# Kernel tuning notes

Measured on AMD Instinct MI355X. Metric: run time of the kernel, lower is better.

The kernel has to match this reference:

```python
import jax, jax.numpy as jnp
import numpy as np

B, L = 1024, 1024
NCAT, NNUM = 20, 10
CAT_BUCKETS, SEQ_VOCAB = 100000, 50000
E, A, H, QH = 32, 128, 256, 256
TOPK = 30


def _init(key, shape, scale=0.02):
    return scale * jax.random.normal(key, shape, dtype=jnp.float32)


def setup_inputs() -> dict:
    key = jax.random.key(0)
    ks = jax.random.split(key, 24)
    z = lambda *s: jnp.zeros(s, dtype=jnp.float32)
    return {
        "cats": jax.random.randint(ks[0], (B, NCAT), 0, CAT_BUCKETS + 1),
        "nums": jax.random.normal(ks[1], (B, NNUM), dtype=jnp.float32),
        "seqs": jax.random.randint(ks[2], (B, L), 0, SEQ_VOCAB + 1),
        "tgt_ids": jax.random.randint(ks[3], (B,), 0, CAT_BUCKETS + 1),
        "cat_emb": _init(ks[4], (CAT_BUCKETS + 1, E)),
        "seq_emb": _init(ks[5], (SEQ_VOCAB + 1, E)),
        "Wnum": _init(ks[6], (NNUM, E)), "bnum": z(E),
        "Wq": _init(ks[7], (E, A)), "Wk": _init(ks[8], (E, A)), "Wv": _init(ks[9], (E, A)),
        "Wo": _init(ks[10], (A, E)), "bo": z(E),
        "Wpool": _init(ks[11], (NCAT * E, E)), "bpool": z(E),
        "Wmlp": _init(ks[12], (4 * E, H)), "bmlp": z(H),
        "q1_W1": _init(ks[13], (H, QH)), "q1_b1": z(QH),
        "q1_W2": _init(ks[14], (H, QH)), "q1_b2": z(QH),
        "q1_Wp": _init(ks[15], (QH, H)), "q1_bp": z(H),
        "q2_W1": _init(ks[16], (H, QH)), "q2_b1": z(QH),
        "q2_W2": _init(ks[17], (H, QH)), "q2_b2": z(QH),
        "q2_Wp": _init(ks[18], (QH, H)), "q2_bp": z(H),
        "Wout": _init(ks[19], (H, 1)), "bout": z(1),
    }


def _qnn(x, W1, b1, W2, b2, Wp, bp):
    # Quadratic neural block (QIN-style): Hadamard product of two linear maps,
    # projected back with a residual connection. Dropout is identity in eval.
    quad = (x @ W1 + b1) * (x @ W2 + b2)
    return x + quad @ Wp + bp


def reference(cats, nums, seqs, tgt_ids, cat_emb, seq_emb, Wnum, bnum, Wq, Wk, Wv,
              Wo, bo, Wpool, bpool, Wmlp, bmlp,
              q1_W1, q1_b1, q1_W2, q1_b2, q1_Wp, q1_bp,
              q2_W1, q2_b1, q2_W2, q2_b2, q2_Wp, q2_bp, Wout, bout):
    cat_e = cat_emb[cats]                                   # [B, NCAT, E]
    cat_pool = cat_e.reshape(cat_e.shape[0], -1) @ Wpool + bpool   # [B, E]
    num_e = nums @ Wnum + bnum                              # [B, E]
    tgt_e = cat_emb[tgt_ids]                                # [B, E] (tgt_emb shares cat_emb)
    seq_e = seq_emb[seqs]                                   # [B, L, E]

    q = tgt_e @ Wq                                          # [B, A]
    k = seq_e @ Wk                                          # [B, L, A]
    v = seq_e @ Wv                                          # [B, L, A]
    scores = jnp.einsum('ba,bla->bl', q, k) / jnp.sqrt(jnp.float32(A))

    # top-k + scatter mask + masked softmax == softmax over the top-k scores,
    # scattered implicitly via gather of the selected values.
    vals, idx = jax.lax.top_k(scores, TOPK)                 # [B, TOPK]
    w = jax.nn.softmax(vals, axis=1)                        # [B, TOPK]
    v_sel = jnp.take_along_axis(v, idx[:, :, None], axis=1)  # [B, TOPK, A]
    interest = jnp.einsum('bk,bka->ba', w, v_sel) @ Wo + bo  # [B, E]

    fused = jnp.concatenate([tgt_e, interest, cat_pool, num_e], axis=1)  # [B, 4E]
    h = jax.nn.relu(fused @ Wmlp + bmlp)                    # [B, H], dropout=eval
    h = _qnn(h, q1_W1, q1_b1, q1_W2, q1_b2, q1_Wp, q1_bp)
    h = _qnn(h, q2_W1, q2_b1, q2_W2, q2_b2, q2_Wp, q2_bp)
    return (h @ Wout + bout)[:, 0]                          # [B]
```

## Files before the change

kernel.cpp:

```cpp
#include <hip/hip_runtime.h>
#include <hip/hip_fp16.h>

#define B_ 1024
#define L_ 1024
#define NCAT_ 20
#define NNUM_ 10
#define E_ 32
#define A_ 128
#define H_ 256
#define TOPK_ 30
#define INV_SQRT_A 0.08838834764831845f

typedef _Float16 half8 __attribute__((ext_vector_type(8)));
typedef float f32x4 __attribute__((ext_vector_type(4)));

__device__ __forceinline__ unsigned sortable(float f) {
    unsigned u = __float_as_uint(f);
    return (u & 0x80000000u) ? ~u : (u | 0x80000000u);
}
__device__ __forceinline__ float unsortable(unsigned s) {
    unsigned u = (s & 0x80000000u) ? (s ^ 0x80000000u) : ~s;
    return __uint_as_float(u);
}
__device__ __forceinline__ half8 cvt_h8(const float4 u, const float4 v) {
    half8 a;
    a[0] = (_Float16)u.x; a[1] = (_Float16)u.y;
    a[2] = (_Float16)u.z; a[3] = (_Float16)u.w;
    a[4] = (_Float16)v.x; a[5] = (_Float16)v.y;
    a[6] = (_Float16)v.z; a[7] = (_Float16)v.w;
    return a;
}

#define K1_GRID 1356
__global__ __launch_bounds__(256) void fused_prep_kernel(
    const int* __restrict__ cats, const float* __restrict__ nums,
    const int* __restrict__ tgt_ids, const float* __restrict__ cat_emb,
    const float* __restrict__ Wnum, const float* __restrict__ bnum,
    const float* __restrict__ Wq, const float* __restrict__ Wk,
    const float* __restrict__ Wv, const float* __restrict__ Wo,
    const float* __restrict__ Wpool, const float* __restrict__ bpool,
    const float* __restrict__ seq_emb, const float* __restrict__ Wmlp,
    const float* __restrict__ q1W1, const float* __restrict__ q1W2,
    const float* __restrict__ q1Wp,
    const float* __restrict__ q2W1, const float* __restrict__ q2W2,
    const float* __restrict__ q2Wp,
    float* __restrict__ p_out, float* __restrict__ fused, float* __restrict__ M,
    __half2* __restrict__ seq_h2,
    __half* __restrict__ WmlpT,
    __half* __restrict__ W1T1, __half* __restrict__ W2T1, __half* __restrict__ WpT1,
    __half* __restrict__ W1T2, __half* __restrict__ W2T2, __half* __restrict__ WpT2)
{
    const int blk = blockIdx.x;
    const int t = threadIdx.x;

    if (blk < 256) {
        __shared__ float ce[4][NCAT_ * E_];
        __shared__ float tg[4][E_];
        __shared__ float nm[4][NNUM_];
        __shared__ float qs[4][A_];
        __shared__ float part[8][4][E_];
        const int r0 = blk * 4;

        for (int idx = t; idx < 640; idx += 256) {
            const int q = idx >> 3, f4 = idx & 7;
            const int row = q / 20, cat = q % 20;
            const int tok = cats[(r0 + row) * NCAT_ + cat];
            ((float4*)&ce[row][cat * 32])[f4] =
                ((const float4*)(cat_emb + (size_t)tok * 32))[f4];
        }
        if (t < 32) {
            const int row = t >> 3, f4 = t & 7;
            const int tok = tgt_ids[r0 + row];
            ((float4*)&tg[row][0])[f4] =
                ((const float4*)(cat_emb + (size_t)tok * 32))[f4];
        }
        if (t >= 64 && t < 104) {
            const int x = t - 64;
            nm[x / 10][x % 10] = nums[(r0 + x / 10) * NNUM_ + x % 10];
        }
        __syncthreads();

        {
            const int w = t >> 6, lane = t & 63;
            float q0 = 0.f, q1 = 0.f;
#pragma unroll
            for (int e = 0; e < E_; ++e) {
                float te = tg[w][e];
                q0 += te * Wq[e * A_ + lane];
                q1 += te * Wq[e * A_ + lane + 64];
            }
            qs[w][lane] = q0; qs[w][lane + 64] = q1;
        }

        {
            const int iseg = t >> 5;
            const int row = (t >> 3) & 3;
            const int c0 = (t & 7) * 4;
            float4 acc = make_float4(0.f, 0.f, 0.f, 0.f);
            const int i0 = iseg * 80;
            for (int i = i0; i < i0 + 80; ++i) {
                float4 wv = *(const float4*)(Wpool + i * 32 + c0);
                acc.x += ce[row][i] * wv.x; acc.y += ce[row][i] * wv.y;
                acc.z += ce[row][i] * wv.z; acc.w += ce[row][i] * wv.w;
            }
            *(float4*)&part[iseg][row][c0] = acc;
        }
        __syncthreads();

        if (t < 128) {
            const int row = t >> 5, c = t & 31;
            const int b = r0 + row;
            float s = bpool[c];
#pragma unroll
            for (int g = 0; g < 8; ++g) s += part[g][row][c];
            fused[b * 128 + 64 + c] = s;
            fused[b * 128 + c] = tg[row][c];

            float ne = bnum[c];
#pragma unroll
            for (int n = 0; n < NNUM_; ++n) ne += nm[row][n] * Wnum[n * 32 + c];
            fused[b * 128 + 96 + c] = ne;

            float pv = 0.f;
#pragma unroll 8
            for (int a = 0; a < A_; ++a) pv += Wk[c * A_ + a] * qs[row][a];
            p_out[b * 32 + c] = pv;
        }
        return;
    }

    if (blk < 1280) {
        int x = (blk - 256) * 256 + t;
        for (; x < 800016; x += 1024 * 256) {
            float2 v = ((const float2*)seq_emb)[x];
            seq_h2[x] = __float22half2_rn(v);
        }
        return;
    }

    if (blk < 1284) {
        const int o = (blk - 1280) * 256 + t;
        const int j = o >> 5, e = o & 31;
        float sm = 0.f;
#pragma unroll 8
        for (int a = 0; a < A_; ++a) sm += Wv[j * A_ + a] * Wo[a * E_ + e];
        M[o] = sm;
        return;
    }

    {
        int c = (blk - 1284) * 256 + t;
        for (; c < 53248; c += 72 * 256) {
            const float* src; __half* dst;
            int n, k0, K;
            if (c < 4096) {
                n = c >> 4; k0 = (c & 15) << 3; K = 128;
                src = Wmlp; dst = WmlpT;
            } else {
                const int c2 = c - 4096;
                const int m = c2 >> 13, idx = c2 & 8191;
                n = idx >> 5; k0 = (idx & 31) << 3; K = 256;
                switch (m) {
                    case 0: src = q1W1; dst = W1T1; break;
                    case 1: src = q1W2; dst = W2T1; break;
                    case 2: src = q1Wp; dst = WpT1; break;
                    case 3: src = q2W1; dst = W1T2; break;
                    case 4: src = q2W2; dst = W2T2; break;
                    default: src = q2Wp; dst = WpT2; break;
                }
            }
            float v[8];
#pragma unroll
            for (int i = 0; i < 8; ++i) v[i] = src[(size_t)(k0 + i) * 256 + n];
            float4 wq;
            __half2* hp = (__half2*)&wq;
            hp[0] = __float22half2_rn(make_float2(v[0], v[1]));
            hp[1] = __float22half2_rn(make_float2(v[2], v[3]));
            hp[2] = __float22half2_rn(make_float2(v[4], v[5]));
            hp[3] = __float22half2_rn(make_float2(v[6], v[7]));
            *(float4*)(dst + (size_t)n * K + k0) = wq;
        }
    }
}

#define RM 2
__global__ __launch_bounds__(512) void score_topk_kernel(
    const int* __restrict__ seqs, const __half* __restrict__ seq_h,
    const float* __restrict__ seq_emb, const float* __restrict__ p,
    const float* __restrict__ M, const float* __restrict__ bo,
    float* __restrict__ fused)
{
    const int b0 = blockIdx.x * RM;
    const int tid = threadIdx.x;

    __shared__ float sc[RM][L_];
    __shared__ float ps[RM][E_];
    __shared__ float sw[RM][32];
    __shared__ int   stok[RM][32];

    if (tid < RM * 32)
        ps[tid >> 5][tid & 31] = p[(b0 + (tid >> 5)) * 32 + (tid & 31)];
    __syncthreads();

    {
        const int row = tid >> 8;
        const int s = tid & 255;
        const int bb = b0 + row;
#pragma unroll
        for (int jj = 0; jj < 2; ++jj) {
            const int l1 = jj * 512 + s;
            const int l2 = l1 + 256;
            const int tok1 = seqs[bb * L_ + l1];
            const int tok2 = seqs[bb * L_ + l2];
            float4 buf[2][4];
            const float4* r1 = (const float4*)(seq_h + (size_t)tok1 * 32);
            const float4* r2 = (const float4*)(seq_h + (size_t)tok2 * 32);
#pragma unroll
            for (int i = 0; i < 4; ++i) buf[0][i] = r1[i];
#pragma unroll
            for (int i = 0; i < 4; ++i) buf[1][i] = r2[i];

            float acc0 = 0.f, acc1 = 0.f;
#pragma unroll
            for (int i = 0; i < 4; ++i) {
                const __half2* h1 = (const __half2*)&buf[0][i];
                const __half2* h2 = (const __half2*)&buf[1][i];
#pragma unroll
                for (int u = 0; u < 4; ++u) {
                    float2 f1 = __half22float2(h1[u]);
                    float2 f2 = __half22float2(h2[u]);
                    acc0 += f1.x * ps[row][i * 8 + 2 * u] + f1.y * ps[row][i * 8 + 2 * u + 1];
                    acc1 += f2.x * ps[row][i * 8 + 2 * u] + f2.y * ps[row][i * 8 + 2 * u + 1];
                }
            }
            sc[row][l1] = acc0 * INV_SQRT_A;
            sc[row][l2] = acc1 * INV_SQRT_A;
        }
    }
    __syncthreads();

    if (tid < RM * 64) {
        const int w = tid >> 6;
        const int lane = tid & 63;
        const int bb = b0 + w;

        unsigned long long key[16];
#pragma unroll
        for (int j = 0; j < 16; ++j) {
            const int l = j * 64 + lane;
            key[j] = ((unsigned long long)sortable(sc[w][l]) << 10)
                   | (unsigned)(1023 - l);
        }
#pragma unroll
        for (int a = 0; a < 15; ++a)
#pragma unroll
            for (int j = 0; j < 15 - a; ++j) {
                const bool swp = key[j] < key[j + 1];
                const unsigned long long hi = swp ? key[j + 1] : key[j];
                const unsigned long long lo = swp ? key[j] : key[j + 1];
                key[j] = hi; key[j + 1] = lo;
            }

        float myv = -1e30f; int myl = 0;
        unsigned long long front = key[0];
        for (int k = 0; k < TOPK_; ++k) {
            unsigned long long wk = front;
#pragma unroll
            for (int off = 32; off > 0; off >>= 1) {
                unsigned long long o = __shfl_xor(wk, off);
                if (o > wk) wk = o;
            }
            if (lane == k) {
                myv = unsortable((unsigned)(wk >> 10));
                myl = 1023 - (int)(wk & 1023);
            }
            if (front == wk) {
#pragma unroll
                for (int j = 0; j < 15; ++j) key[j] = key[j + 1];
                key[15] = 0ULL;
                front = key[0];
            }
        }

        float m = myv;
#pragma unroll
        for (int off = 32; off > 0; off >>= 1) m = fmaxf(m, __shfl_xor(m, off));
        float e = (lane < TOPK_) ? expf(myv - m) : 0.f;
        float s = e;
#pragma unroll
        for (int off = 32; off > 0; off >>= 1) s += __shfl_xor(s, off);
        if (lane < TOPK_) {
            sw[w][lane]   = e / s;
            stok[w][lane] = seqs[bb * L_ + myl];
        }

        if (lane < E_) {
            float acc = 0.f;
#pragma unroll
            for (int k = 0; k < TOPK_; ++k)
                acc += sw[w][k] * seq_emb[(size_t)stok[w][k] * 32 + lane];
            sc[w][lane] = acc;
        }
        if (lane < E_) {
            float acc = bo[lane];
#pragma unroll
            for (int j = 0; j < E_; ++j) acc += sc[w][j] * M[j * E_ + lane];
            fused[bb * 128 + 32 + lane] = acc;
        }
    }
}

#define GR 16
#define HSP 260
#define TSP 264
__global__ __launch_bounds__(512) void mlp_mfma_kernel(
    const float* __restrict__ fused,
    const __half* __restrict__ WmlpT, const float* __restrict__ bmlp,
    const __half* __restrict__ W1T1, const __half* __restrict__ W2T1,
    const __half* __restrict__ WpT1,
    const float* __restrict__ b11, const float* __restrict__ b12,
    const float* __restrict__ b1p,
    const __half* __restrict__ W1T2, const __half* __restrict__ W2T2,
    const __half* __restrict__ WpT2,
    const float* __restrict__ b21, const float* __restrict__ b22,
    const float* __restrict__ b2p,
    const float* __restrict__ Wout, const float* __restrict__ bout,
    float* __restrict__ out)
{
    const int r0 = blockIdx.x * GR;
    const int tid = threadIdx.x;
    const int w = tid >> 6;
    const int l = tid & 63;
    const int lr = l & 15;
    const int lk = l >> 4;
    const int n0 = w * 32;

    __shared__ float hs[GR][HSP];
    __shared__ __half ts_h[GR][TSP];

    f32x4 hC0, hC1;
    const f32x4 zf = {0.f, 0.f, 0.f, 0.f};

    {
        half8 ax[4];
        const float* xrow = fused + (size_t)(r0 + lr) * 128 + lk * 8;
#pragma unroll
        for (int ks = 0; ks < 4; ++ks) {
            float4 u = *(const float4*)(xrow + ks * 32);
            float4 v = *(const float4*)(xrow + ks * 32 + 4);
            ax[ks] = cvt_h8(u, v);
        }
#pragma unroll
        for (int t = 0; t < 2; ++t) {
            f32x4 c = zf;
            const __half* wb = WmlpT + (size_t)(n0 + 16 * t + lr) * 128 + lk * 8;
#pragma unroll
            for (int ks = 0; ks < 4; ++ks) {
                half8 b = *(const half8*)(wb + ks * 32);
                c = __builtin_amdgcn_mfma_f32_16x16x32_f16(ax[ks], b, c, 0, 0, 0);
            }
            const int j = n0 + 16 * t + lr;
            const float bm = bmlp[j];
#pragma unroll
            for (int r = 0; r < 4; ++r) {
                float vv = fmaxf(c[r] + bm, 0.f);
                if (t == 0) hC0[r] = vv; else hC1[r] = vv;
                hs[4 * lk + r][j] = vv;
            }
        }
    }
    __syncthreads();

#pragma unroll
    for (int q = 0; q < 2; ++q) {
        const __half* W1T = q ? W1T2 : W1T1;
        const __half* W2T = q ? W2T2 : W2T1;
        const __half* WpT = q ? WpT2 : WpT1;
        const float* bb1 = q ? b21 : b11;
        const float* bb2 = q ? b22 : b12;
        const float* bbp = q ? b2p : b1p;

        half8 ah[8];
#pragma unroll
        for (int ks = 0; ks < 8; ++ks) {
            const float* hr = &hs[lr][ks * 32 + lk * 8];
            float4 u = *(const float4*)hr;
            float4 v = *(const float4*)(hr + 4);
            ah[ks] = cvt_h8(u, v);
        }
#pragma unroll
        for (int t = 0; t < 2; ++t) {
            f32x4 t1 = zf, t2 = zf;
            const __half* w1 = W1T + (size_t)(n0 + 16 * t + lr) * 256 + lk * 8;
            const __half* w2 = W2T + (size_t)(n0 + 16 * t + lr) * 256 + lk * 8;
#pragma unroll
            for (int ks = 0; ks < 8; ++ks) {
                half8 b1 = *(const half8*)(w1 + ks * 32);
                t1 = __builtin_amdgcn_mfma_f32_16x16x32_f16(ah[ks], b1, t1, 0, 0, 0);
                half8 b2 = *(const half8*)(w2 + ks * 32);
                t2 = __builtin_amdgcn_mfma_f32_16x16x32_f16(ah[ks], b2, t2, 0, 0, 0);
            }
            const int j = n0 + 16 * t + lr;
            const float v1 = bb1[j], v2 = bb2[j];
#pragma unroll
            for (int r = 0; r < 4; ++r) {
                float tv = (t1[r] + v1) * (t2[r] + v2);
                ts_h[4 * lk + r][j] = __float2half_rn(tv);
            }
        }
        __syncthreads();

        half8 pa[8];
#pragma unroll
        for (int ks = 0; ks < 8; ++ks)
            pa[ks] = *(const half8*)&ts_h[lr][ks * 32 + lk * 8];
#pragma unroll
        for (int t = 0; t < 2; ++t) {
            f32x4 c = (t == 0) ? hC0 : hC1;
            const __half* wp = WpT + (size_t)(n0 + 16 * t + lr) * 256 + lk * 8;
#pragma unroll
            for (int ks = 0; ks < 8; ++ks) {
                half8 b = *(const half8*)(wp + ks * 32);
                c = __builtin_amdgcn_mfma_f32_16x16x32_f16(pa[ks], b, c, 0, 0, 0);
            }
            const int j = n0 + 16 * t + lr;
            const float bp = bbp[j];
#pragma unroll
            for (int r = 0; r < 4; ++r) {
                float vv = c[r] + bp;
                if (t == 0) hC0[r] = vv; else hC1[r] = vv;
                hs[4 * lk + r][j] = vv;
            }
        }
        __syncthreads();
    }

    {
        const int i = tid >> 5;
        const int seg = tid & 31;
        const int cb = seg * 8;
        float psum = 0.f;
#pragma unroll
        for (int u = 0; u < 8; ++u) psum += hs[i][cb + u] * Wout[cb + u];
#pragma unroll
        for (int off = 16; off > 0; off >>= 1) psum += __shfl_xor(psum, off);
        if (seg == 0) out[r0 + i] = psum + bout[0];
    }
}

extern "C" void kernel_launch(void* const* d_in, const int* in_sizes, int n_in,
                              void* d_out, int out_size, void* d_ws, size_t ws_size,
                              hipStream_t stream) {
    const int*   cats    = (const int*)d_in[0];
    const float* nums    = (const float*)d_in[1];
    const int*   seqs    = (const int*)d_in[2];
    const int*   tgt_ids = (const int*)d_in[3];
    const float* cat_emb = (const float*)d_in[4];
    const float* seq_emb = (const float*)d_in[5];
    const float* Wnum    = (const float*)d_in[6];
    const float* bnum    = (const float*)d_in[7];
    const float* Wq      = (const float*)d_in[8];
    const float* Wk      = (const float*)d_in[9];
    const float* Wv      = (const float*)d_in[10];
    const float* Wo      = (const float*)d_in[11];
    const float* bo      = (const float*)d_in[12];
    const float* Wpool   = (const float*)d_in[13];
    const float* bpool   = (const float*)d_in[14];
    const float* Wmlp    = (const float*)d_in[15];
    const float* bmlp    = (const float*)d_in[16];
    const float* q1_W1   = (const float*)d_in[17];
    const float* q1_b1   = (const float*)d_in[18];
    const float* q1_W2   = (const float*)d_in[19];
    const float* q1_b2   = (const float*)d_in[20];
    const float* q1_Wp   = (const float*)d_in[21];
    const float* q1_bp   = (const float*)d_in[22];
    const float* q2_W1   = (const float*)d_in[23];
    const float* q2_b1   = (const float*)d_in[24];
    const float* q2_W2   = (const float*)d_in[25];
    const float* q2_b2   = (const float*)d_in[26];
    const float* q2_Wp   = (const float*)d_in[27];
    const float* q2_bp   = (const float*)d_in[28];
    const float* Wout    = (const float*)d_in[29];
    const float* bout    = (const float*)d_in[30];

    float* ws = (float*)d_ws;
    float*   p       = ws;
    float*   fused   = ws + 32768;
    float*   M       = ws + 163840;
    __half2* seq_h2  = (__half2*)(ws + 164864);
    __half*  WmlpT   = (__half*)(ws + 964928);
    __half*  W1T1    = (__half*)(ws + 981312);
    __half*  W2T1    = (__half*)(ws + 1014080);
    __half*  WpT1    = (__half*)(ws + 1046848);
    __half*  W1T2    = (__half*)(ws + 1079616);
    __half*  W2T2    = (__half*)(ws + 1112384);
    __half*  WpT2    = (__half*)(ws + 1145152);

    float* out = (float*)d_out;

    fused_prep_kernel<<<K1_GRID, 256, 0, stream>>>(
        cats, nums, tgt_ids, cat_emb, Wnum, bnum, Wq, Wk, Wv, Wo,
        Wpool, bpool, seq_emb, Wmlp,
        q1_W1, q1_W2, q1_Wp, q2_W1, q2_W2, q2_Wp,
        p, fused, M, seq_h2,
        WmlpT, W1T1, W2T1, WpT1, W1T2, W2T2, WpT2);

    score_topk_kernel<<<B_ / RM, 512, 0, stream>>>(
        seqs, (const __half*)seq_h2, seq_emb, p, M, bo, fused);

    mlp_mfma_kernel<<<B_ / GR, 512, 0, stream>>>(
        fused, WmlpT, bmlp,
        W1T1, W2T1, WpT1, q1_b1, q1_b2, q1_bp,
        W1T2, W2T2, WpT2, q2_b1, q2_b2, q2_bp,
        Wout, bout, out);
}
```

Baseline: 200.6 us.

## Drop fp16 seq table conversion and fuse score/top-k with MLP via last-block counter

Removes the per-call fp32-to-fp16 conversion of the whole sequence embedding table and has the score kernel read fp32 rows directly. It also merges the score/top-k kernel with the MLP kernel: each group of four blocks increments an atomic counter, and the last block to arrive runs the MFMA MLP for its 16 rows. The intent is to avoid converting the full table when only the gathered rows are used, and to save one kernel launch. In exchange, gathers are now twice as wide, and the MLP runs on only a quarter of the blocks, serialized behind the counter.

New measurement: 219.1 us. +9.2%, slower.

```diff
diff --git a/kernel.cpp b/kernel.cpp
--- a/kernel.cpp
+++ b/kernel.cpp
@@ -31,7 +31,7 @@
     return a;
 }
 
-#define K1_GRID 1356
+#define K1_GRID 332
 __global__ __launch_bounds__(256) void fused_prep_kernel(
     const int* __restrict__ cats, const float* __restrict__ nums,
     const int* __restrict__ tgt_ids, const float* __restrict__ cat_emb,
@@ -39,13 +39,13 @@
     const float* __restrict__ Wq, const float* __restrict__ Wk,
     const float* __restrict__ Wv, const float* __restrict__ Wo,
     const float* __restrict__ Wpool, const float* __restrict__ bpool,
-    const float* __restrict__ seq_emb, const float* __restrict__ Wmlp,
+    const float* __restrict__ Wmlp,
     const float* __restrict__ q1W1, const float* __restrict__ q1W2,
     const float* __restrict__ q1Wp,
     const float* __restrict__ q2W1, const float* __restrict__ q2W2,
     const float* __restrict__ q2Wp,
     float* __restrict__ p_out, float* __restrict__ fused, float* __restrict__ M,
-    __half2* __restrict__ seq_h2,
+    int* __restrict__ cnt,
     __half* __restrict__ WmlpT,
     __half* __restrict__ W1T1, __half* __restrict__ W2T1, __half* __restrict__ WpT1,
     __half* __restrict__ W1T2, __half* __restrict__ W2T2, __half* __restrict__ WpT2)
@@ -76,7 +76,7 @@
         }
         if (t >= 64 && t < 104) {
             const int x = t - 64;
-            nm[x / 10][x % 10] = nums[(r0 + x / 10) * NNUM_ + x % 10];
+            nm[x / 10][x % 10] = nums[(x / 10) * 0 + (r0 + x / 10) * NNUM_ + x % 10];
         }
         __syncthreads();
 
@@ -129,17 +129,9 @@
         return;
     }
 
-    if (blk < 1280) {
-        int x = (blk - 256) * 256 + t;
-        for (; x < 800016; x += 1024 * 256) {
-            float2 v = ((const float2*)seq_emb)[x];
-            seq_h2[x] = __float22half2_rn(v);
-        }
-        return;
-    }
-
-    if (blk < 1284) {
-        const int o = (blk - 1280) * 256 + t;
+    if (blk < 260) {
+        if (blk == 256 && t < 64) cnt[t] = 0;
+        const int o = (blk - 256) * 256 + t;
         const int j = o >> 5, e = o & 31;
         float sm = 0.f;
 #pragma unroll 8
@@ -149,7 +141,7 @@
     }
 
     {
-        int c = (blk - 1284) * 256 + t;
+        int c = (blk - 260) * 256 + t;
         for (; c < 53248; c += 72 * 256) {
             const float* src; __half* dst;
             int n, k0, K;
@@ -183,138 +175,15 @@
     }
 }
 
-#define RM 2
-__global__ __launch_bounds__(512) void score_topk_kernel(
-    const int* __restrict__ seqs, const __half* __restrict__ seq_h,
-    const float* __restrict__ seq_emb, const float* __restrict__ p,
-    const float* __restrict__ M, const float* __restrict__ bo,
-    float* __restrict__ fused)
-{
-    const int b0 = blockIdx.x * RM;
-    const int tid = threadIdx.x;
-
-    __shared__ float sc[RM][L_];
-    __shared__ float ps[RM][E_];
-    __shared__ float sw[RM][32];
-    __shared__ int   stok[RM][32];
-
-    if (tid < RM * 32)
-        ps[tid >> 5][tid & 31] = p[(b0 + (tid >> 5)) * 32 + (tid & 31)];
-    __syncthreads();
-
-    {
-        const int row = tid >> 8;
-        const int s = tid & 255;
-        const int bb = b0 + row;
-#pragma unroll
-        for (int jj = 0; jj < 2; ++jj) {
-            const int l1 = jj * 512 + s;
-            const int l2 = l1 + 256;
-            const int tok1 = seqs[bb * L_ + l1];
-            const int tok2 = seqs[bb * L_ + l2];
-            float4 buf[2][4];
-            const float4* r1 = (const float4*)(seq_h + (size_t)tok1 * 32);
-            const float4* r2 = (const float4*)(seq_h + (size_t)tok2 * 32);
-#pragma unroll
-            for (int i = 0; i < 4; ++i) buf[0][i] = r1[i];
-#pragma unroll
-            for (int i = 0; i < 4; ++i) buf[1][i] = r2[i];
-
-            float acc0 = 0.f, acc1 = 0.f;
-#pragma unroll
-            for (int i = 0; i < 4; ++i) {
-                const __half2* h1 = (const __half2*)&buf[0][i];
-                const __half2* h2 = (const __half2*)&buf[1][i];
-#pragma unroll
-                for (int u = 0; u < 4; ++u) {
-                    float2 f1 = __half22float2(h1[u]);
-                    float2 f2 = __half22float2(h2[u]);
-                    acc0 += f1.x * ps[row][i * 8 + 2 * u] + f1.y * ps[row][i * 8 + 2 * u + 1];
-                    acc1 += f2.x * ps[row][i * 8 + 2 * u] + f2.y * ps[row][i * 8 + 2 * u + 1];
-                }
-            }
-            sc[row][l1] = acc0 * INV_SQRT_A;
-            sc[row][l2] = acc1 * INV_SQRT_A;
-        }
-    }
-    __syncthreads();
-
-    if (tid < RM * 64) {
-        const int w = tid >> 6;
-        const int lane = tid & 63;
-        const int bb = b0 + w;
-
-        unsigned long long key[16];
-#pragma unroll
-        for (int j = 0; j < 16; ++j) {
-            const int l = j * 64 + lane;
-            key[j] = ((unsigned long long)sortable(sc[w][l]) << 10)
-                   | (unsigned)(1023 - l);
-        }
-#pragma unroll
-        for (int a = 0; a < 15; ++a)
-#pragma unroll
-            for (int j = 0; j < 15 - a; ++j) {
-                const bool swp = key[j] < key[j + 1];
-                const unsigned long long hi = swp ? key[j + 1] : key[j];
-                const unsigned long long lo = swp ? key[j] : key[j + 1];
-                key[j] = hi; key[j + 1] = lo;
-            }
-
-        float myv = -1e30f; int myl = 0;
-        unsigned long long front = key[0];
-        for (int k = 0; k < TOPK_; ++k) {
-            unsigned long long wk = front;
-#pragma unroll
-            for (int off = 32; off > 0; off >>= 1) {
-                unsigned long long o = __shfl_xor(wk, off);
-                if (o > wk) wk = o;
-            }
-            if (lane == k) {
-                myv = unsortable((unsigned)(wk >> 10));
-                myl = 1023 - (int)(wk & 1023);
-            }
-            if (front == wk) {
-#pragma unroll
-                for (int j = 0; j < 15; ++j) key[j] = key[j + 1];
-                key[15] = 0ULL;
-                front = key[0];
-            }
-        }
-
-        float m = myv;
-#pragma unroll
-        for (int off = 32; off > 0; off >>= 1) m = fmaxf(m, __shfl_xor(m, off));
-        float e = (lane < TOPK_) ? expf(myv - m) : 0.f;
-        float s = e;
-#pragma unroll
-        for (int off = 32; off > 0; off >>= 1) s += __shfl_xor(s, off);
-        if (lane < TOPK_) {
-            sw[w][lane]   = e / s;
-            stok[w][lane] = seqs[bb * L_ + myl];
-        }
-
-        if (lane < E_) {
-            float acc = 0.f;
-#pragma unroll
-            for (int k = 0; k < TOPK_; ++k)
-                acc += sw[w][k] * seq_emb[(size_t)stok[w][k] * 32 + lane];
-            sc[w][lane] = acc;
-        }
-        if (lane < E_) {
-            float acc = bo[lane];
-#pragma unroll
-            for (int j = 0; j < E_; ++j) acc += sc[w][j] * M[j * E_ + lane];
-            fused[bb * 128 + 32 + lane] = acc;
-        }
-    }
-}
-
+#define RM 4
 #define GR 16
 #define HSP 260
 #define TSP 264
-__global__ __launch_bounds__(512) void mlp_mfma_kernel(
-    const float* __restrict__ fused,
+__global__ __launch_bounds__(512) void score_mlp_kernel(
+    const int* __restrict__ seqs, const float* __restrict__ seq_emb,
+    const float* __restrict__ p, const float* __restrict__ M,
+    const float* __restrict__ bo, float* __restrict__ fused,
+    int* __restrict__ cnt,
     const __half* __restrict__ WmlpT, const float* __restrict__ bmlp,
     const __half* __restrict__ W1T1, const __half* __restrict__ W2T1,
     const __half* __restrict__ WpT1,
@@ -327,23 +196,146 @@
     const float* __restrict__ Wout, const float* __restrict__ bout,
     float* __restrict__ out)
 {
-    const int r0 = blockIdx.x * GR;
+    const int b0 = blockIdx.x * RM;
     const int tid = threadIdx.x;
+
+    __shared__ float sc[RM][L_];
+    __shared__ float ps[RM][E_];
+    __shared__ float sw[RM][32];
+    __shared__ int   stok[RM][32];
+    __shared__ float hs[GR][HSP];
+    __shared__ __half ts_h[GR][TSP];
+    __shared__ int doml;
+
+    if (tid < RM * 32)
+        ps[tid >> 5][tid & 31] = p[(b0 + (tid >> 5)) * 32 + (tid & 31)];
+    __syncthreads();
+
+    {
+        const int row = tid >> 7;
+        const int s = tid & 127;
+        const int base = (b0 + row) * L_;
+#pragma unroll
+        for (int jj = 0; jj < 4; ++jj) {
+            const int l1 = jj * 128 + s;
+            const int l2 = l1 + 512;
+            const int tok1 = seqs[base + l1];
+            const int tok2 = seqs[base + l2];
+            const float4* r1 = (const float4*)(seq_emb + (size_t)tok1 * 32);
+            const float4* r2 = (const float4*)(seq_emb + (size_t)tok2 * 32);
+            float4 bufA[8], bufB[8];
+#pragma unroll
+            for (int i = 0; i < 8; ++i) bufA[i] = r1[i];
+#pragma unroll
+            for (int i = 0; i < 8; ++i) bufB[i] = r2[i];
+            float a0 = 0.f, a1 = 0.f;
+#pragma unroll
+            for (int i = 0; i < 8; ++i) {
+                a0 += bufA[i].x * ps[row][4 * i]     + bufA[i].y * ps[row][4 * i + 1]
+                    + bufA[i].z * ps[row][4 * i + 2] + bufA[i].w * ps[row][4 * i + 3];
+                a1 += bufB[i].x * ps[row][4 * i]     + bufB[i].y * ps[row][4 * i + 1]
+                    + bufB[i].z * ps[row][4 * i + 2] + bufB[i].w * ps[row][4 * i + 3];
+            }
+            sc[row][l1] = a0 * INV_SQRT_A;
+            sc[row][l2] = a1 * INV_SQRT_A;
+        }
+    }
+    __syncthreads();
+
+    if (tid < RM * 64) {
+        const int w = tid >> 6;
+        const int lane = tid & 63;
+        const int bb = b0 + w;
+
+        unsigned long long key[16];
+#pragma unroll
+        for (int j = 0; j < 16; ++j) {
+            const int l = j * 64 + lane;
+            key[j] = ((unsigned long long)sortable(sc[w][l]) << 10)
+                   | (unsigned)(1023 - l);
+        }
+#pragma unroll
+        for (int a = 0; a < 15; ++a)
+#pragma unroll
+            for (int j = 0; j < 15 - a; ++j) {
+                const bool swp = key[j] < key[j + 1];
+                const unsigned long long hi = swp ? key[j + 1] : key[j];
+                const unsigned long long lo = swp ? key[j] : key[j + 1];
+                key[j] = hi; key[j + 1] = lo;
+            }
+
+        float myv = -1e30f; int myl = 0;
+        unsigned long long front = key[0];
+        for (int k = 0; k < TOPK_; ++k) {
+            unsigned long long wk = front;
+#pragma unroll
+            for (int off = 32; off > 0; off >>= 1) {
+                unsigned long long o = __shfl_xor(wk, off);
+                if (o > wk) wk = o;
+            }
+            if (lane == k) {
+                myv = unsortable((unsigned)(wk >> 10));
+                myl = 1023 - (int)(wk & 1023);
+            }
+            if (front == wk) {
+#pragma unroll
+                for (int j = 0; j < 15; ++j) key[j] = key[j + 1];
+                key[15] = 0ULL;
+                front = key[0];
+            }
+        }
+
+        float m = myv;
+#pragma unroll
+        for (int off = 32; off > 0; off >>= 1) m = fmaxf(m, __shfl_xor(m, off));
+        float e = (lane < TOPK_) ? expf(myv - m) : 0.f;
+        float s = e;
+#pragma unroll
+        for (int off = 32; off > 0; off >>= 1) s += __shfl_xor(s, off);
+        if (lane < TOPK_) {
+            sw[w][lane]   = e / s;
+            stok[w][lane] = seqs[bb * L_ + myl];
+        }
+
+        if (lane < E_) {
+            float acc = 0.f;
+#pragma unroll
+            for (int k = 0; k < TOPK_; ++k)
+                acc += sw[w][k] * seq_emb[(size_t)stok[w][k] * 32 + lane];
+            sc[w][lane] = acc;
+        }
+        if (lane < E_) {
+            float acc = bo[lane];
+#pragma unroll
+            for (int j = 0; j < E_; ++j) acc += sc[w][j] * M[j * E_ + lane];
+            fused[bb * 128 + 32 + lane] = acc;
+        }
+    }
+    __syncthreads();
+
+    if (tid == 0) {
+        __threadfence();
+        const int g = blockIdx.x >> 2;
+        const int old = atomicAdd(&cnt[g], 1);
+        doml = (old == 3) ? 1 : 0;
+        if (old == 3) __threadfence();
+    }
+    __syncthreads();
+    if (!doml) return;
+
+    const int r0m = (blockIdx.x >> 2) * GR;
     const int w = tid >> 6;
     const int l = tid & 63;
     const int lr = l & 15;
     const int lk = l >> 4;
     const int n0 = w * 32;
 
-    __shared__ float hs[GR][HSP];
-    __shared__ __half ts_h[GR][TSP];
-
     f32x4 hC0, hC1;
     const f32x4 zf = {0.f, 0.f, 0.f, 0.f};
 
     {
         half8 ax[4];
-        const float* xrow = fused + (size_t)(r0 + lr) * 128 + lk * 8;
+        const float* xrow = fused + (size_t)(r0m + lr) * 128 + lk * 8;
 #pragma unroll
         for (int ks = 0; ks < 4; ++ks) {
             float4 u = *(const float4*)(xrow + ks * 32);
@@ -444,7 +436,7 @@
         for (int u = 0; u < 8; ++u) psum += hs[i][cb + u] * Wout[cb + u];
 #pragma unroll
         for (int off = 16; off > 0; off >>= 1) psum += __shfl_xor(psum, off);
-        if (seg == 0) out[r0 + i] = psum + bout[0];
+        if (seg == 0) out[r0m + i] = psum + bout[0];
     }
 }
 
@@ -487,29 +479,27 @@
     float*   p       = ws;
     float*   fused   = ws + 32768;
     float*   M       = ws + 163840;
-    __half2* seq_h2  = (__half2*)(ws + 164864);
-    __half*  WmlpT   = (__half*)(ws + 964928);
-    __half*  W1T1    = (__half*)(ws + 981312);
-    __half*  W2T1    = (__half*)(ws + 1014080);
-    __half*  WpT1    = (__half*)(ws + 1046848);
-    __half*  W1T2    = (__half*)(ws + 1079616);
-    __half*  W2T2    = (__half*)(ws + 1112384);
-    __half*  WpT2    = (__half*)(ws + 1145152);
+    int*     cnt     = (int*)(ws + 164864);
+    __half*  WmlpT   = (__half*)(ws + 164928);
+    __half*  W1T1    = (__half*)(ws + 181312);
+    __half*  W2T1    = (__half*)(ws + 214080);
+    __half*  WpT1    = (__half*)(ws + 246848);
+    __half*  W1T2    = (__half*)(ws + 279616);
+    __half*  W2T2    = (__half*)(ws + 312384);
+    __half*  WpT2    = (__half*)(ws + 345152);
 
     float* out = (float*)d_out;
 
     fused_prep_kernel<<<K1_GRID, 256, 0, stream>>>(
         cats, nums, tgt_ids, cat_emb, Wnum, bnum, Wq, Wk, Wv, Wo,
-        Wpool, bpool, seq_emb, Wmlp,
+        Wpool, bpool, Wmlp,
         q1_W1, q1_W2, q1_Wp, q2_W1, q2_W2, q2_Wp,
-        p, fused, M, seq_h2,
+        p, fused, M, cnt,
         WmlpT, W1T1, W2T1, WpT1, W1T2, W2T2, WpT2);
 
-    score_topk_kernel<<<B_ / RM, 512, 0, stream>>>(
-        seqs, (const __half*)seq_h2, seq_emb, p, M, bo, fused);
-
-    mlp_mfma_kernel<<<B_ / GR, 512, 0, stream>>>(
-        fused, WmlpT, bmlp,
+    score_mlp_kernel<<<B_ / RM, 512, 0, stream>>>(
+        seqs, seq_emb, p, M, bo, fused, cnt,
+        WmlpT, bmlp,
         W1T1, W2T1, WpT1, q1_b1, q1_b2, q1_bp,
         W1T2, W2T2, WpT2, q2_b1, q2_b2, q2_bp,
         Wout, bout, out);
```

## Fuse score/top-k and MLP kernels via last-block-arrives atomic counter

Applied to the files above, without the earlier changes.

Merges the score/top-k kernel and the MFMA MLP kernel into one launch. Each block now handles 4 rows instead of 2, and a per-group atomic counter, zeroed in the prep kernel, lets the last of 4 blocks run the 16-row MLP tile. This removes one kernel launch and the gap between the two kernels. In exchange, the MLP tail runs on only a quarter of the blocks, and the fused kernel's larger shared-memory footprint may lower occupancy during the score phase.

Result: no change. 199.3 us (-0.7%).

```diff
diff --git a/kernel.cpp b/kernel.cpp
--- a/kernel.cpp
+++ b/kernel.cpp
@@ -45,7 +45,7 @@
     const float* __restrict__ q2W1, const float* __restrict__ q2W2,
     const float* __restrict__ q2Wp,
     float* __restrict__ p_out, float* __restrict__ fused, float* __restrict__ M,
-    __half2* __restrict__ seq_h2,
+    int* __restrict__ cnt, __half2* __restrict__ seq_h2,
     __half* __restrict__ WmlpT,
     __half* __restrict__ W1T1, __half* __restrict__ W2T1, __half* __restrict__ WpT1,
     __half* __restrict__ W1T2, __half* __restrict__ W2T2, __half* __restrict__ WpT2)
@@ -139,6 +139,7 @@
     }
 
     if (blk < 1284) {
+        if (blk == 1280 && t < 64) cnt[t] = 0;
         const int o = (blk - 1280) * 256 + t;
         const int j = o >> 5, e = o & 31;
         float sm = 0.f;
@@ -183,138 +184,15 @@
     }
 }
 
-#define RM 2
-__global__ __launch_bounds__(512) void score_topk_kernel(
+#define RM 4
+#define GR 16
+#define HSP 260
+#define TSP 264
+__global__ __launch_bounds__(512) void score_mlp_kernel(
     const int* __restrict__ seqs, const __half* __restrict__ seq_h,
     const float* __restrict__ seq_emb, const float* __restrict__ p,
     const float* __restrict__ M, const float* __restrict__ bo,
-    float* __restrict__ fused)
-{
-    const int b0 = blockIdx.x * RM;
-    const int tid = threadIdx.x;
-
-    __shared__ float sc[RM][L_];
-    __shared__ float ps[RM][E_];
-    __shared__ float sw[RM][32];
-    __shared__ int   stok[RM][32];
-
-    if (tid < RM * 32)
-        ps[tid >> 5][tid & 31] = p[(b0 + (tid >> 5)) * 32 + (tid & 31)];
-    __syncthreads();
-
-    {
-        const int row = tid >> 8;
-        const int s = tid & 255;
-        const int bb = b0 + row;
-#pragma unroll
-        for (int jj = 0; jj < 2; ++jj) {
-            const int l1 = jj * 512 + s;
-            const int l2 = l1 + 256;
-            const int tok1 = seqs[bb * L_ + l1];
-            const int tok2 = seqs[bb * L_ + l2];
-            float4 buf[2][4];
-            const float4* r1 = (const float4*)(seq_h + (size_t)tok1 * 32);
-            const float4* r2 = (const float4*)(seq_h + (size_t)tok2 * 32);
-#pragma unroll
-            for (int i = 0; i < 4; ++i) buf[0][i] = r1[i];
-#pragma unroll
-            for (int i = 0; i < 4; ++i) buf[1][i] = r2[i];
-
-            float acc0 = 0.f, acc1 = 0.f;
-#pragma unroll
-            for (int i = 0; i < 4; ++i) {
-                const __half2* h1 = (const __half2*)&buf[0][i];
-                const __half2* h2 = (const __half2*)&buf[1][i];
-#pragma unroll
-                for (int u = 0; u < 4; ++u) {
-                    float2 f1 = __half22float2(h1[u]);
-                    float2 f2 = __half22float2(h2[u]);
-                    acc0 += f1.x * ps[row][i * 8 + 2 * u] + f1.y * ps[row][i * 8 + 2 * u + 1];
-                    acc1 += f2.x * ps[row][i * 8 + 2 * u] + f2.y * ps[row][i * 8 + 2 * u + 1];
-                }
-            }
-            sc[row][l1] = acc0 * INV_SQRT_A;
-            sc[row][l2] = acc1 * INV_SQRT_A;
-        }
-    }
-    __syncthreads();
-
-    if (tid < RM * 64) {
-        const int w = tid >> 6;
-        const int lane = tid & 63;
-        const int bb = b0 + w;
-
-        unsigned long long key[16];
-#pragma unroll
-        for (int j = 0; j < 16; ++j) {
-            const int l = j * 64 + lane;
-            key[j] = ((unsigned long long)sortable(sc[w][l]) << 10)
-                   | (unsigned)(1023 - l);
-        }
-#pragma unroll
-        for (int a = 0; a < 15; ++a)
-#pragma unroll
-            for (int j = 0; j < 15 - a; ++j) {
-                const bool swp = key[j] < key[j + 1];
-                const unsigned long long hi = swp ? key[j + 1] : key[j];
-                const unsigned long long lo = swp ? key[j] : key[j + 1];
-                key[j] = hi; key[j + 1] = lo;
-            }
-
-        float myv = -1e30f; int myl = 0;
-        unsigned long long front = key[0];
-        for (int k = 0; k < TOPK_; ++k) {
-            unsigned long long wk = front;
-#pragma unroll
-            for (int off = 32; off > 0; off >>= 1) {
-                unsigned long long o = __shfl_xor(wk, off);
-                if (o > wk) wk = o;
-            }
-            if (lane == k) {
-                myv = unsortable((unsigned)(wk >> 10));
-                myl = 1023 - (int)(wk & 1023);
-            }
-            if (front == wk) {
-#pragma unroll
-                for (int j = 0; j < 15; ++j) key[j] = key[j + 1];
-                key[15] = 0ULL;
-                front = key[0];
-            }
-        }
-
-        float m = myv;
-#pragma unroll
-        for (int off = 32; off > 0; off >>= 1) m = fmaxf(m, __shfl_xor(m, off));
-        float e = (lane < TOPK_) ? expf(myv - m) : 0.f;
-        float s = e;
-#pragma unroll
-        for (int off = 32; off > 0; off >>= 1) s += __shfl_xor(s, off);
-        if (lane < TOPK_) {
-            sw[w][lane]   = e / s;
-            stok[w][lane] = seqs[bb * L_ + myl];
-        }
-
-        if (lane < E_) {
-            float acc = 0.f;
-#pragma unroll
-            for (int k = 0; k < TOPK_; ++k)
-                acc += sw[w][k] * seq_emb[(size_t)stok[w][k] * 32 + lane];
-            sc[w][lane] = acc;
-        }
-        if (lane < E_) {
-            float acc = bo[lane];
-#pragma unroll
-            for (int j = 0; j < E_; ++j) acc += sc[w][j] * M[j * E_ + lane];
-            fused[bb * 128 + 32 + lane] = acc;
-        }
-    }
-}
-
-#define GR 16
-#define HSP 260
-#define TSP 264
-__global__ __launch_bounds__(512) void mlp_mfma_kernel(
-    const float* __restrict__ fused,
+    float* __restrict__ fused, int* __restrict__ cnt,
     const __half* __restrict__ WmlpT, const float* __restrict__ bmlp,
     const __half* __restrict__ W1T1, const __half* __restrict__ W2T1,
     const __half* __restrict__ WpT1,
@@ -327,23 +205,152 @@
     const float* __restrict__ Wout, const float* __restrict__ bout,
     float* __restrict__ out)
 {
-    const int r0 = blockIdx.x * GR;
+    const int b0 = blockIdx.x * RM;
     const int tid = threadIdx.x;
+
+    __shared__ float sc[RM][L_];
+    __shared__ float ps[RM][E_];
+    __shared__ float sw[RM][32];
+    __shared__ int   stok[RM][32];
+    __shared__ float hs[GR][HSP];
+    __shared__ __half ts_h[GR][TSP];
+    __shared__ int doml;
+
+    if (tid < RM * 32)
+        ps[tid >> 5][tid & 31] = p[(b0 + (tid >> 5)) * 32 + (tid & 31)];
+    __syncthreads();
+
+    {
+        const int row = tid >> 7;
+        const int s = tid & 127;
+        const int bb = b0 + row;
+#pragma unroll
+        for (int jj = 0; jj < 4; ++jj) {
+            const int l1 = jj * 256 + s;
+            const int l2 = l1 + 128;
+            const int tok1 = seqs[bb * L_ + l1];
+            const int tok2 = seqs[bb * L_ + l2];
+            float4 buf[2][4];
+            const float4* r1 = (const float4*)(seq_h + (size_t)tok1 * 32);
+            const float4* r2 = (const float4*)(seq_h + (size_t)tok2 * 32);
+#pragma unroll
+            for (int i = 0; i < 4; ++i) buf[0][i] = r1[i];
+#pragma unroll
+            for (int i = 0; i < 4; ++i) buf[1][i] = r2[i];
+
+            float acc0 = 0.f, acc1 = 0.f;
+#pragma unroll
+            for (int i = 0; i < 4; ++i) {
+                const __half2* h1 = (const __half2*)&buf[0][i];
+                const __half2* h2 = (const __half2*)&buf[1][i];
+#pragma unroll
+                for (int u = 0; u < 4; ++u) {
+                    float2 f1 = __half22float2(h1[u]);
+                    float2 f2 = __half22float2(h2[u]);
+                    acc0 += f1.x * ps[row][i * 8 + 2 * u] + f1.y * ps[row][i * 8 + 2 * u + 1];
+                    acc1 += f2.x * ps[row][i * 8 + 2 * u] + f2.y * ps[row][i * 8 + 2 * u + 1];
+                }
+            }
+            sc[row][l1] = acc0 * INV_SQRT_A;
+            sc[row][l2] = acc1 * INV_SQRT_A;
+        }
+    }
+    __syncthreads();
+
+    if (tid < RM * 64) {
+        const int w = tid >> 6;
+        const int lane = tid & 63;
+        const int bb = b0 + w;
+
+        unsigned long long key[16];
+#pragma unroll
+        for (int j = 0; j < 16; ++j) {
+            const int l = j * 64 + lane;
+            key[j] = ((unsigned long long)sortable(sc[w][l]) << 10)
+                   | (unsigned)(1023 - l);
+        }
+#pragma unroll
+        for (int a = 0; a < 15; ++a)
+#pragma unroll
+            for (int j = 0; j < 15 - a; ++j) {
+                const bool swp = key[j] < key[j + 1];
+                const unsigned long long hi = swp ? key[j + 1] : key[j];
+                const unsigned long long lo = swp ? key[j] : key[j + 1];
+                key[j] = hi; key[j + 1] = lo;
+            }
+
+        float myv = -1e30f; int myl = 0;
+        unsigned long long front = key[0];
+        for (int k = 0; k < TOPK_; ++k) {
+            unsigned long long wk = front;
+#pragma unroll
+            for (int off = 32; off > 0; off >>= 1) {
+                unsigned long long o = __shfl_xor(wk, off);
+                if (o > wk) wk = o;
+            }
+            if (lane == k) {
+                myv = unsortable((unsigned)(wk >> 10));
+                myl = 1023 - (int)(wk & 1023);
+            }
+            if (front == wk) {
+#pragma unroll
+                for (int j = 0; j < 15; ++j) key[j] = key[j + 1];
+                key[15] = 0ULL;
+                front = key[0];
+            }
+        }
+
+        float m = myv;
+#pragma unroll
+        for (int off = 32; off > 0; off >>= 1) m = fmaxf(m, __shfl_xor(m, off));
+        float e = (lane < TOPK_) ? expf(myv - m) : 0.f;
+        float s = e;
+#pragma unroll
+        for (int off = 32; off > 0; off >>= 1) s += __shfl_xor(s, off);
+        if (lane < TOPK_) {
+            sw[w][lane]   = e / s;
+            stok[w][lane] = seqs[bb * L_ + myl];
+        }
+
+        if (lane < E_) {
+            float acc = 0.f;
+#pragma unroll
+            for (int k = 0; k < TOPK_; ++k)
+                acc += sw[w][k] * seq_emb[(size_t)stok[w][k] * 32 + lane];
+            sc[w][lane] = acc;
+        }
+        if (lane < E_) {
+            float acc = bo[lane];
+#pragma unroll
+            for (int j = 0; j < E_; ++j) acc += sc[w][j] * M[j * E_ + lane];
+            fused[bb * 128 + 32 + lane] = acc;
+        }
+    }
+    __syncthreads();
+
+    if (tid == 0) {
+        __threadfence();
+        const int g = blockIdx.x >> 2;
+        const int old = atomicAdd(&cnt[g], 1);
+        doml = (old == 3) ? 1 : 0;
+        if (old == 3) __threadfence();
+    }
+    __syncthreads();
+    if (!doml) return;
+
+    const int r0m = (blockIdx.x >> 2) * GR;
     const int w = tid >> 6;
     const int l = tid & 63;
     const int lr = l & 15;
     const int lk = l >> 4;
     const int n0 = w * 32;
 
-    __shared__ float hs[GR][HSP];
-    __shared__ __half ts_h[GR][TSP];
-
     f32x4 hC0, hC1;
     const f32x4 zf = {0.f, 0.f, 0.f, 0.f};
 
     {
         half8 ax[4];
-        const float* xrow = fused + (size_t)(r0 + lr) * 128 + lk * 8;
+        const float* xrow = fused + (size_t)(r0m + lr) * 128 + lk * 8;
 #pragma unroll
         for (int ks = 0; ks < 4; ++ks) {
             float4 u = *(const float4*)(xrow + ks * 32);
@@ -444,7 +451,7 @@
         for (int u = 0; u < 8; ++u) psum += hs[i][cb + u] * Wout[cb + u];
 #pragma unroll
         for (int off = 16; off > 0; off >>= 1) psum += __shfl_xor(psum, off);
-        if (seg == 0) out[r0 + i] = psum + bout[0];
+        if (seg == 0) out[r0m + i] = psum + bout[0];
     }
 }
 
@@ -487,14 +494,15 @@
     float*   p       = ws;
     float*   fused   = ws + 32768;
     float*   M       = ws + 163840;
-    __half2* seq_h2  = (__half2*)(ws + 164864);
-    __half*  WmlpT   = (__half*)(ws + 964928);
-    __half*  W1T1    = (__half*)(ws + 981312);
-    __half*  W2T1    = (__half*)(ws + 1014080);
-    __half*  WpT1    = (__half*)(ws + 1046848);
-    __half*  W1T2    = (__half*)(ws + 1079616);
-    __half*  W2T2    = (__half*)(ws + 1112384);
-    __half*  WpT2    = (__half*)(ws + 1145152);
+    int*     cnt     = (int*)(ws + 164864);
+    __half2* seq_h2  = (__half2*)(ws + 164928);
+    __half*  WmlpT   = (__half*)(ws + 964992);
+    __half*  W1T1    = (__half*)(ws + 981376);
+    __half*  W2T1    = (__half*)(ws + 1014144);
+    __half*  WpT1    = (__half*)(ws + 1046912);
+    __half*  W1T2    = (__half*)(ws + 1079680);
+    __half*  W2T2    = (__half*)(ws + 1112448);
+    __half*  WpT2    = (__half*)(ws + 1145216);
 
     float* out = (float*)d_out;
 
@@ -502,14 +510,12 @@
         cats, nums, tgt_ids, cat_emb, Wnum, bnum, Wq, Wk, Wv, Wo,
         Wpool, bpool, seq_emb, Wmlp,
         q1_W1, q1_W2, q1_Wp, q2_W1, q2_W2, q2_Wp,
-        p, fused, M, seq_h2,
+        p, fused, M, cnt, seq_h2,
         WmlpT, W1T1, W2T1, WpT1, W1T2, W2T2, WpT2);
 
-    score_topk_kernel<<<B_ / RM, 512, 0, stream>>>(
-        seqs, (const __half*)seq_h2, seq_emb, p, M, bo, fused);
-
-    mlp_mfma_kernel<<<B_ / GR, 512, 0, stream>>>(
-        fused, WmlpT, bmlp,
+    score_mlp_kernel<<<B_ / RM, 512, 0, stream>>>(
+        seqs, (const __half*)seq_h2, seq_emb, p, M, bo, fused, cnt,
+        WmlpT, bmlp,
         W1T1, W2T1, WpT1, q1_b1, q1_b2, q1_bp,
         W1T2, W2T2, WpT2, q2_b1, q2_b2, q2_bp,
         Wout, bout, out);
```
